# Kernel tuning notes

Measured on AMD Instinct MI355X. Metric: run time of the kernel, lower is better.

The kernel has to match this reference:

```python
import jax, jax.numpy as jnp
import numpy as np

B, N, DIM, H, CH, M = 2, 65536, 256, 8, 32, 64
INNER = H * CH  # 256


def setup_inputs() -> dict:
    key = jax.random.key(0)
    ks = jax.random.split(key, 13)
    s = 0.02
    return {
        "x": jax.random.normal(ks[0], (B, N, DIM), dtype=jnp.float32),
        "W_fx": jax.random.normal(ks[1], (DIM, INNER), dtype=jnp.float32) * s,
        "b_fx": jnp.zeros((INNER,), dtype=jnp.float32),
        "W_x": jax.random.normal(ks[2], (DIM, INNER), dtype=jnp.float32) * s,
        "b_x": jnp.zeros((INNER,), dtype=jnp.float32),
        "W_slice": jax.random.normal(ks[3], (CH, M), dtype=jnp.float32) * s,
        "b_slice": jnp.zeros((M,), dtype=jnp.float32),
        "temperature": 0.5 * jnp.ones((1, H, 1, 1), dtype=jnp.float32),
        "W_q": jax.random.normal(ks[4], (CH, CH), dtype=jnp.float32) * s,
        "W_k": jax.random.normal(ks[5], (CH, CH), dtype=jnp.float32) * s,
        "W_v": jax.random.normal(ks[6], (CH, CH), dtype=jnp.float32) * s,
        "W_out": jax.random.normal(ks[7], (INNER, DIM), dtype=jnp.float32) * s,
        "b_out": jnp.zeros((DIM,), dtype=jnp.float32),
    }


def reference(x, W_fx, b_fx, W_x, b_x, W_slice, b_slice, temperature,
              W_q, W_k, W_v, W_out, b_out):
    b, n, _ = x.shape
    h, ch, m = H, CH, M
    # input projections -> [B, H, N, Ch]
    fx_mid = (x @ W_fx + b_fx).reshape(b, n, h, ch).transpose(0, 2, 1, 3)
    x_mid = (x @ W_x + b_x).reshape(b, n, h, ch).transpose(0, 2, 1, 3)
    # learned soft-slice weights: [B, H, N, M]
    temp = jnp.clip(temperature, 0.1, 5.0)
    logits = (x_mid @ W_slice + b_slice) / temp
    slice_weights = jax.nn.softmax(logits, axis=-1)
    slice_norm = slice_weights.sum(axis=2)  # [B, H, M]
    # aggregate N points into M slice tokens: [B, H, M, Ch]
    slice_token = jnp.einsum('bhnc,bhng->bhgc', fx_mid, slice_weights)
    slice_token = slice_token / (slice_norm + 1e-5)[:, :, :, None]
    # small attention among slice tokens
    q = slice_token @ W_q
    k = slice_token @ W_k
    v = slice_token @ W_v
    scale = ch ** (-0.5)
    attn = jax.nn.softmax(jnp.einsum('bhgc,bhkc->bhgk', q, k) * scale, axis=-1)
    out_slice = attn @ v  # [B, H, M, Ch]
    # scatter back to N points: [B, H, N, Ch] -> [B, N, H*Ch]
    out_x = jnp.einsum('bhgc,bhng->bhnc', out_slice, slice_weights)
    out_x = out_x.transpose(0, 2, 1, 3).reshape(b, n, h * ch)
    return out_x @ W_out + b_out
```

## Files before the change

### kernel.cpp

```cpp
#include <hip/hip_runtime.h>

#define N_ 65536

typedef unsigned int  uint32;
typedef unsigned short ushort;
typedef float  f32x4 __attribute__((ext_vector_type(4)));
typedef short  s16x8 __attribute__((ext_vector_type(8)));
typedef uint32 u32x2 __attribute__((ext_vector_type(2)));

__device__ __forceinline__ uint32 f2bf(float f){
  union{float f; uint32 i;} v; v.f=f;
  return (v.i + 0x7fffu + ((v.i>>16)&1u)) >> 16;
}
__device__ __forceinline__ float bfl(uint32 h){
  union{uint32 i; float f;} v; v.i = h<<16; return v.f;
}
__device__ __forceinline__ uint32 pk2(float a, float b){
  return f2bf(a) | (f2bf(b)<<16);
}
__device__ __forceinline__ f32x4 mfma16(s16x8 a, s16x8 b, f32x4 c){
  return __builtin_amdgcn_mfma_f32_16x16x32_bf16(a,b,c,0,0,0);
}

__global__ __launch_bounds__(256) void prep_kernel(
    const float* __restrict__ Wfx, const float* __restrict__ Wx,
    const float* __restrict__ Wsl, const float* __restrict__ bsl,
    const float* __restrict__ bx,  const float* __restrict__ temp,
    ushort* __restrict__ WlT, ushort* __restrict__ WfxT, float* __restrict__ blT)
{
  const int blk = blockIdx.x, t = threadIdx.x;
  if (blk < 512){
    const int m = blk, h = m>>6, mp = m&63;
    const float tmp = fminf(fmaxf(temp[h],0.1f),5.0f);
    float s = 0.f;
    #pragma unroll
    for (int cc=0; cc<32; cc++) s += Wx[t*256 + h*32+cc]*Wsl[cc*64+mp];
    WlT[m*256+t] = (ushort)f2bf(s/tmp);
    if (t==0){
      float bs = bsl[mp];
      for (int cc=0; cc<32; cc++) bs += bx[h*32+cc]*Wsl[cc*64+mp];
      blT[m] = bs/tmp;
    }
  } else {
    const int c = blk-512;
    WfxT[c*256+t] = (ushort)f2bf(Wfx[t*256+c]);
  }
}

__global__ __launch_bounds__(512, 2)
void k1a_kernel(
    const float* __restrict__ x,
    const ushort* __restrict__ WlT,
    const ushort* __restrict__ WfxT,
    const float* __restrict__ blT,
    const float* __restrict__ bfx,
    ushort* __restrict__ swg,
    float* __restrict__ stp,
    float* __restrict__ normp)
{
  __shared__ __align__(16) char smem[131072];
  const int t = threadIdx.x;
  const int w = t>>6, l = t&63, rg = l>>4, c16 = l&15;
  const int blk = blockIdx.x;
  const int tile0 = ((blk&127)<<3) + ((blk>>7)<<10);

  char* fxh = smem + (w<<12);
  char* swb = smem + 32768 + (w<<13);
  char* fxl = smem + 98304 + (w<<12);

  f32x4 pc[2][4];
  #pragma unroll
  for (int i=0;i<2;i++)
    #pragma unroll
    for (int j=0;j<4;j++) pc[i][j] = (f32x4){0.f,0.f,0.f,0.f};
  f32x4 nacc[4];
  #pragma unroll
  for (int i=0;i<4;i++) nacc[i] = (f32x4){0.f,0.f,0.f,0.f};

  f32x4 blv[4];
  #pragma unroll
  for (int m=0;m<4;m++) blv[m] = *(const f32x4*)(blT + (w<<6)+(m<<4)+(rg<<2));
  float bfv[2];
  #pragma unroll
  for (int c=0;c<2;c++) bfv[c] = bfx[(w<<5)+(c<<4)+c16];

  for (int it=0; it<8; ++it) {
    const int tile = tile0 + it;
    const long gn0 = (long)tile<<6;

    __syncthreads();
    {
      const float4* xs = (const float4*)(x + (gn0<<8));
      #pragma unroll
      for (int p=0;p<8;p++){
        const int f = t + (p<<9);
        const int row = f>>6, q = f&63;
        const float4 v = xs[f];
        u32x2 uu; uu.x = pk2(v.x, v.y); uu.y = pk2(v.z, v.w);
        *(u32x2*)(smem + (row<<9) + ((q<<3) ^ ((row&7)<<4))) = uu;
      }
    }
    __syncthreads();

    #pragma unroll
    for (int nf=0; nf<4; nf++){
      f32x4 accA[4];
      #pragma unroll
      for (int m=0;m<4;m++) accA[m] = (f32x4){0.f,0.f,0.f,0.f};
      #pragma unroll
      for (int kb=0;kb<8;kb++){
        s16x8 aW[4], bX;
        #pragma unroll
        for (int m=0;m<4;m++)
          aW[m] = *(const s16x8*)(WlT + (((w<<6)+(m<<4)+c16)<<8) + (kb<<5)+(rg<<3));
        {
          const int row = (nf<<4) | c16;
          bX = *(const s16x8*)(smem + (row<<9) + (((kb<<6)+(rg<<4)) ^ ((row&7)<<4)));
        }
        #pragma unroll
        for (int m=0;m<4;m++)
          accA[m] = mfma16(aW[m], bX, accA[m]);
      }
      {
        f32x4 v[4];
        float mx = -3.0e38f;
        #pragma unroll
        for (int m=0;m<4;m++){
          v[m] = accA[m] + blv[m];
          mx = fmaxf(mx, fmaxf(fmaxf(v[m].x, v[m].y), fmaxf(v[m].z, v[m].w)));
        }
        mx = fmaxf(mx, __shfl_xor(mx,16));
        mx = fmaxf(mx, __shfl_xor(mx,32));
        float s = 0.f;
        #pragma unroll
        for (int m=0;m<4;m++){
          v[m].x = __expf(v[m].x-mx); v[m].y = __expf(v[m].y-mx);
          v[m].z = __expf(v[m].z-mx); v[m].w = __expf(v[m].w-mx);
          s += v[m].x+v[m].y+v[m].z+v[m].w;
        }
        s += __shfl_xor(s,16);
        s += __shfl_xor(s,32);
        const float inv = 1.0f/s;
        const long gn = gn0 + (nf<<4) + c16;
        #pragma unroll
        for (int m=0;m<4;m++){
          f32x4 sv = v[m]*inv;
          nacc[m] += sv;
          u32x2 p; p.x = pk2(sv.x, sv.y); p.y = pk2(sv.z, sv.w);
          *(u32x2*)(swg + (gn<<9) + (w<<6)+(m<<4)+(rg<<2)) = p;
          const uint32 px = (uint32)__shfl_xor((int)p.x, 1);
          const uint32 py = (uint32)__shfl_xor((int)p.y, 1);
          const bool ev = ((c16&1)==0);
          const uint32 s0 = ev ? (uint32)p.x : py;
          const uint32 s1 = ev ? px : (uint32)p.y;
          const uint32 wA = (s0 & 0xffffu) | (s1<<16);
          const uint32 wB = (s0>>16) | (s1 & 0xffff0000u);
          const int rowA = (m<<4) + (rg<<2) + (ev?0:2);
          const int cbyt = ((nf<<4) + (c16 & ~1)) << 1;
          *(uint32*)(swb + ((rowA  )<<7) + (cbyt ^ (((rowA  )&7)<<4))) = wA;
          *(uint32*)(swb + ((rowA+1)<<7) + (cbyt ^ (((rowA+1)&7)<<4))) = wB;
        }
      }
    }

    u32x2 qkh[2][4];
    {
      f32x4 accB[4][2];
      #pragma unroll
      for (int r=0;r<4;r++)
        #pragma unroll
        for (int c=0;c<2;c++) accB[r][c] = (f32x4){0.f,0.f,0.f,0.f};
      #pragma unroll
      for (int kb=0;kb<8;kb++){
        s16x8 bW[2], aX[4];
        #pragma unroll
        for (int c=0;c<2;c++)
          bW[c] = *(const s16x8*)(WfxT + (((w<<5)+(c<<4)+c16)<<8) + (kb<<5)+(rg<<3));
        #pragma unroll
        for (int r=0;r<4;r++){
          const int row = (r<<4) | c16;
          aX[r] = *(const s16x8*)(smem + (row<<9) + (((kb<<6)+(rg<<4)) ^ ((row&7)<<4)));
        }
        #pragma unroll
        for (int r=0;r<4;r++)
          #pragma unroll
          for (int c=0;c<2;c++)
            accB[r][c] = mfma16(aX[r], bW[c], accB[r][c]);
      }
      #pragma unroll
      for (int r=0;r<4;r++)
        #pragma unroll
        for (int c=0;c<2;c++){
          const float v0 = accB[r][c].x+bfv[c], v1 = accB[r][c].y+bfv[c];
          const float v2 = accB[r][c].z+bfv[c], v3 = accB[r][c].w+bfv[c];
          const uint32 h0=f2bf(v0), h1=f2bf(v1), h2=f2bf(v2), h3=f2bf(v3);
          u32x2 ph; ph.x = h0|(h1<<16); ph.y = h2|(h3<<16);
          qkh[c][r] = ph;
          u32x2 pl;
          pl.x = f2bf(v0-bfl(h0)) | (f2bf(v1-bfl(h1))<<16);
          pl.y = f2bf(v2-bfl(h2)) | (f2bf(v3-bfl(h3))<<16);
          const int row = (c<<4) + c16;
          const int cby = ((r<<5) + (rg<<3)) ^ ((row&7)<<4);
          *(u32x2*)(fxl + (row<<7) + cby) = pl;
        }
    }
    __syncthreads();

    #pragma unroll
    for (int cf=0; cf<2; cf++)
      #pragma unroll
      for (int r=0; r<4; r++){
        const int row = (cf<<4) + c16;
        const int cby = ((r<<5) + (rg<<3)) ^ ((row&7)<<4);
        *(u32x2*)(fxh + (row<<7) + cby) = qkh[cf][r];
      }
    asm volatile("s_waitcnt lgkmcnt(0)" ::: "memory");
    __builtin_amdgcn_sched_barrier(0);

    #pragma unroll
    for (int kb2=0; kb2<2; kb2++){
      const int pby = (kb2<<6) + (rg<<4);
      s16x8 afh[2], afl[2], bfr[4];
      #pragma unroll
      for (int cf=0; cf<2; cf++){
        const int row = (cf<<4)+c16;
        const int o = pby ^ ((row&7)<<4);
        afh[cf] = *(const s16x8*)(fxh + (row<<7) + o);
        afl[cf] = *(const s16x8*)(fxl + (row<<7) + o);
      }
      #pragma unroll
      for (int mf=0; mf<4; mf++){
        const int row = (mf<<4)+c16;
        bfr[mf] = *(const s16x8*)(swb + (row<<7) + (pby ^ ((row&7)<<4)));
      }
      #pragma unroll
      for (int cf=0; cf<2; cf++)
        #pragma unroll
        for (int mf=0; mf<4; mf++){
          pc[cf][mf] = mfma16(afh[cf], bfr[mf], pc[cf][mf]);
          pc[cf][mf] = mfma16(afl[cf], bfr[mf], pc[cf][mf]);
        }
    }
  }

  #pragma unroll
  for (int m=0;m<4;m++){
    #pragma unroll
    for (int d=1; d<16; d<<=1){
      nacc[m].x += __shfl_xor(nacc[m].x, d);
      nacc[m].y += __shfl_xor(nacc[m].y, d);
      nacc[m].z += __shfl_xor(nacc[m].z, d);
      nacc[m].w += __shfl_xor(nacc[m].w, d);
    }
  }
  if (c16==0){
    #pragma unroll
    for (int m=0;m<4;m++)
      *(f32x4*)(normp + (((blk<<3)+w)<<6) + (m<<4) + (rg<<2)) = nacc[m];
  }
  const long sb = ((long)((blk<<3)+w))<<11;
  #pragma unroll
  for (int cf=0;cf<2;cf++)
    #pragma unroll
    for (int mf=0;mf<4;mf++)
      #pragma unroll
      for (int r=0;r<4;r++){
        const int cc = (cf<<4)+(rg<<2)+r;
        stp[sb + (cc<<6) + (mf<<4) + c16] = pc[cf][mf][r];
      }
}

__global__ __launch_bounds__(256) void k2a_kernel(float* __restrict__ stp, float* __restrict__ normp)
{
  const int gid = blockIdx.x;
  const int bh = gid>>3, grp = gid&7;
  const int b = bh>>3, h = bh&7;
  const int t = threadIdx.x;
  const int blk0 = (b<<7) + (grp<<4);
  f32x4 a0 = {0,0,0,0}, a1 = {0,0,0,0};
  for (int i=0;i<16;i++){
    const f32x4* p = (const f32x4*)(stp + ((((size_t)(blk0+i)<<3)+h)<<11) + ((size_t)t<<3));
    a0 += p[0]; a1 += p[1];
  }
  f32x4* q = (f32x4*)(stp + ((((size_t)blk0<<3)+h)<<11) + ((size_t)t<<3));
  q[0] = a0; q[1] = a1;
  if (t<8){
    f32x4 n0 = {0,0,0,0}, n1 = {0,0,0,0};
    for (int i=0;i<16;i++){
      const f32x4* p = (const f32x4*)(normp + (((blk0+i)<<3)+h)*64 + (t<<3));
      n0 += p[0]; n1 += p[1];
    }
    f32x4* qn = (f32x4*)(normp + ((blk0<<3)+h)*64 + (t<<3));
    qn[0] = n0; qn[1] = n1;
  }
}

__global__ __launch_bounds__(256) void k2b_kernel(
    const float* __restrict__ stp, const float* __restrict__ normp,
    const float* __restrict__ Wq, const float* __restrict__ Wk, const float* __restrict__ Wv,
    const float* __restrict__ Wout, ushort* __restrict__ OS2Th, ushort* __restrict__ OS2Tl)
{
  __shared__ float nrmL[64];
  __shared__ float tok[2048];
  __shared__ float qL[2048], kL[2048], vL[2048];
  __shared__ float sc[4096];
  __shared__ float osL[2048];
  const int bh = blockIdx.x; const int b = bh>>3, h = bh&7;
  const int t = threadIdx.x;

  if (t<64){
    float s = 0.f;
    for (int g=0; g<8; g++) s += normp[((((b<<7)+(g<<4))<<3)+h)*64 + t];
    nrmL[t] = s;
  }
  __syncthreads();
  {
    f32x4 a0 = {0,0,0,0}, a1 = {0,0,0,0};
    for (int g=0; g<8; g++){
      const f32x4* p = (const f32x4*)(stp + ((((size_t)((b<<7)+(g<<4))<<3)+h)<<11) + ((size_t)t<<3));
      a0 += p[0]; a1 += p[1];
    }
    const int c = t>>3, m0 = (t&7)<<3;
    #pragma unroll
    for (int j=0;j<4;j++) tok[(m0+j)*32 + c]   = a0[j] / (nrmL[m0+j]   + 1e-5f);
    #pragma unroll
    for (int j=0;j<4;j++) tok[(m0+4+j)*32 + c] = a1[j] / (nrmL[m0+4+j] + 1e-5f);
  }
  __syncthreads();

  const int g = t>>2, q4 = t&3;
  float aq[8]={0,0,0,0,0,0,0,0}, ak2[8]={0,0,0,0,0,0,0,0}, av[8]={0,0,0,0,0,0,0,0};
  for (int kk=0; kk<32; kk++){
    const float tv = tok[(g<<5)+kk];
    const int wo = kk*32 + (q4<<3);
    #pragma unroll
    for (int j=0;j<8;j++){
      aq[j]  = fmaf(tv, Wq[wo+j], aq[j]);
      ak2[j] = fmaf(tv, Wk[wo+j], ak2[j]);
      av[j]  = fmaf(tv, Wv[wo+j], av[j]);
    }
  }
  #pragma unroll
  for (int j=0;j<8;j++){
    qL[(g<<5)+(q4<<3)+j]=aq[j];
    kL[(g<<5)+(q4<<3)+j]=ak2[j];
    vL[(g<<5)+(q4<<3)+j]=av[j];
  }
  __syncthreads();

  const float scale = 0.17677669529663689f;
  float svv[16]; float mx = -3.0e38f;
  for (int mm=0;mm<16;mm++){
    const int m = (q4<<4)+mm;
    float s2 = 0.f;
    #pragma unroll
    for (int c=0;c<32;c++) s2 = fmaf(qL[(g<<5)+c], kL[(m<<5)+c], s2);
    s2 *= scale;
    svv[mm] = s2; mx = fmaxf(mx, s2);
  }
  mx = fmaxf(mx, __shfl_xor(mx,1));
  mx = fmaxf(mx, __shfl_xor(mx,2));
  float ssum = 0.f;
  for (int mm=0;mm<16;mm++){ svv[mm] = __expf(svv[mm]-mx); ssum += svv[mm]; }
  ssum += __shfl_xor(ssum,1); ssum += __shfl_xor(ssum,2);
  const float isum = 1.0f/ssum;
  for (int mm=0;mm<16;mm++) sc[(g<<6) + (q4<<4) + mm] = svv[mm]*isum;
  __syncthreads();

  float os[8]={0,0,0,0,0,0,0,0};
  for (int m=0;m<64;m++){
    const float a = sc[(g<<6)+m];
    const int vo = (m<<5)+(q4<<3);
    #pragma unroll
    for (int j=0;j<8;j++) os[j] = fmaf(a, vL[vo+j], os[j]);
  }
  #pragma unroll
  for (int j=0;j<8;j++) osL[(g<<5)+(q4<<3)+j] = os[j];
  __syncthreads();

  const int d = t;
  float wcol[32];
  #pragma unroll
  for (int c=0;c<32;c++) wcol[c] = Wout[(h*32+c)*256 + d];
  uint32* orh = (uint32*)(OS2Th + ((size_t)(b*256+d))*512 + h*64);
  uint32* orl = (uint32*)(OS2Tl + ((size_t)(b*256+d))*512 + h*64);
  #pragma unroll 4
  for (int g2=0; g2<32; g2++){
    float s0=0.f, s1=0.f;
    #pragma unroll
    for (int c=0;c<32;c++){
      s0 = fmaf(osL[((g2*2  )<<5)+c], wcol[c], s0);
      s1 = fmaf(osL[((g2*2+1)<<5)+c], wcol[c], s1);
    }
    const uint32 h0 = f2bf(s0), h1 = f2bf(s1);
    orh[g2] = h0 | (h1<<16);
    orl[g2] = f2bf(s0 - bfl(h0)) | (f2bf(s1 - bfl(h1)) << 16);
  }
}

__global__ __launch_bounds__(256) void k3_kernel(
    const ushort* __restrict__ swg,
    const ushort* __restrict__ OS2Th,
    const ushort* __restrict__ OS2Tl,
    const float* __restrict__ bout,
    float* __restrict__ out)
{
  const int t = threadIdx.x, w = t>>6, l = t&63, rg = l>>4, c16 = l&15;
  const int blk = blockIdx.x;
  const long gn0 = (long)blk<<7;
  const int b = blk>>9;
  f32x4 acc[8][4];
  #pragma unroll
  for (int r=0;r<8;r++)
    #pragma unroll
    for (int c=0;c<4;c++) acc[r][c] = (f32x4){0.f,0.f,0.f,0.f};
  const ushort* swp = swg + (gn0<<9);
  const long obb = (((long)(b<<8) + (w<<6))<<9);
  for (int kb=0;kb<16;kb++){
    s16x8 aS[8];
    #pragma unroll
    for (int r=0;r<8;r++)
      aS[r] = *(const s16x8*)(swp + ((long)((r<<4)+c16)<<9) + (kb<<5)+(rg<<3));
    #pragma unroll
    for (int c=0;c<4;c++){
      const long ro = obb + ((long)((c<<4)+c16)<<9) + (kb<<5)+(rg<<3);
      const s16x8 bh = *(const s16x8*)(OS2Th + ro);
      const s16x8 bl = *(const s16x8*)(OS2Tl + ro);
      #pragma unroll
      for (int r=0;r<8;r++)
        acc[r][c] = mfma16(aS[r], bh, acc[r][c]);
      #pragma unroll
      for (int r=0;r<8;r++)
        acc[r][c] = mfma16(aS[r], bl, acc[r][c]);
    }
  }
  float bo[4];
  #pragma unroll
  for (int c=0;c<4;c++) bo[c] = bout[(w<<6)+(c<<4)+c16];
  #pragma unroll
  for (int r=0;r<8;r++)
    #pragma unroll
    for (int c=0;c<4;c++)
      #pragma unroll
      for (int rr=0;rr<4;rr++)
        out[((gn0 + (r<<4)+(rg<<2)+rr)<<8) + (w<<6)+(c<<4)+c16] = acc[r][c][rr] + bo[c];
}

extern "C" void kernel_launch(void* const* d_in, const int* in_sizes, int n_in,
                              void* d_out, int out_size, void* d_ws, size_t ws_size,
                              hipStream_t stream)
{
  const float* x     = (const float*)d_in[0];
  const float* Wfx   = (const float*)d_in[1];
  const float* bfx   = (const float*)d_in[2];
  const float* Wx    = (const float*)d_in[3];
  const float* bx    = (const float*)d_in[4];
  const float* Wsl   = (const float*)d_in[5];
  const float* bsl   = (const float*)d_in[6];
  const float* temp  = (const float*)d_in[7];
  const float* Wq    = (const float*)d_in[8];
  const float* Wk    = (const float*)d_in[9];
  const float* Wv    = (const float*)d_in[10];
  const float* Wout  = (const float*)d_in[11];
  const float* bout  = (const float*)d_in[12];
  float* out = (float*)d_out;

  char* ws = (char*)d_ws;
  ushort* WlT   = (ushort*)(ws);
  ushort* WfxT  = (ushort*)(ws + 262144);
  float*  blT   = (float*) (ws + 393216);
  ushort* swg   = (ushort*)(ws + 395264);
  float*  stp   = (float*) (ws + 134612992);
  float*  normp = (float*) (ws + 151390208);
  ushort* OS2Th = (ushort*)(ws + 151914496);
  ushort* OS2Tl = (ushort*)(ws + 152438784);

  prep_kernel<<<dim3(768), dim3(256), 0, stream>>>(Wfx, Wx, Wsl, bsl, bx, temp, WlT, WfxT, blT);
  k1a_kernel<<<dim3(256), dim3(512), 0, stream>>>(x, WlT, WfxT, blT, bfx, swg, stp, normp);
  k2a_kernel<<<dim3(128), dim3(256), 0, stream>>>(stp, normp);
  k2b_kernel<<<dim3(16), dim3(256), 0, stream>>>(stp, normp, Wq, Wk, Wv, Wout, OS2Th, OS2Tl);
  k3_kernel<<<dim3(1024), dim3(256), 0, stream>>>(swg, OS2Th, OS2Tl, bout, out);
}
```

Baseline: 449.9 us.

## Store slice weights in packed tile layout and halve k3 rows per block

The slice-weight buffer written by k1a is rearranged from a row-major [n][512] layout into 16-point packets grouped by head and slice block. Each 8-byte store from a wave then lands in contiguous memory, and k3 can fetch its MFMA A operands as two adjacent 8-byte loads. k3 now covers 64 rows per block with half the accumulators and launches twice as many blocks, aiming at better occupancy and coalescing. The trade-off is that each OS2T B tile is reloaded by twice as many blocks.

```diff
diff --git a/kernel.cpp b/kernel.cpp
--- a/kernel.cpp
+++ b/kernel.cpp
@@ -7,6 +7,7 @@
 typedef float  f32x4 __attribute__((ext_vector_type(4)));
 typedef short  s16x8 __attribute__((ext_vector_type(8)));
 typedef uint32 u32x2 __attribute__((ext_vector_type(2)));
+typedef uint32 u32x4 __attribute__((ext_vector_type(4)));
 
 __device__ __forceinline__ uint32 f2bf(float f){
   union{float f; uint32 i;} v; v.f=f;
@@ -20,6 +21,9 @@
 }
 __device__ __forceinline__ f32x4 mfma16(s16x8 a, s16x8 b, f32x4 c){
   return __builtin_amdgcn_mfma_f32_16x16x32_bf16(a,b,c,0,0,0);
+}
+__device__ __forceinline__ s16x8 mk8(uint32 a, uint32 b, uint32 c, uint32 d){
+  union{u32x4 u; s16x8 s;} v; v.u = (u32x4){a,b,c,d}; return v.s;
 }
 
 __global__ __launch_bounds__(256) void prep_kernel(
@@ -54,7 +58,7 @@
     const ushort* __restrict__ WfxT,
     const float* __restrict__ blT,
     const float* __restrict__ bfx,
-    ushort* __restrict__ swg,
+    ushort* __restrict__ swg2,
     float* __restrict__ stp,
     float* __restrict__ normp)
 {
@@ -141,13 +145,13 @@
         s += __shfl_xor(s,16);
         s += __shfl_xor(s,32);
         const float inv = 1.0f/s;
-        const long gn = gn0 + (nf<<4) + c16;
+        const int pb = (int)(gn0>>4) + nf;
         #pragma unroll
         for (int m=0;m<4;m++){
           f32x4 sv = v[m]*inv;
           nacc[m] += sv;
           u32x2 p; p.x = pk2(sv.x, sv.y); p.y = pk2(sv.z, sv.w);
-          *(u32x2*)(swg + (gn<<9) + (w<<6)+(m<<4)+(rg<<2)) = p;
+          *(u32x2*)(swg2 + ((((((size_t)pb<<3)+w)<<2)+m)<<8) + (rg<<6) + (c16<<2)) = p;
           const uint32 px = (uint32)__shfl_xor((int)p.x, 1);
           const uint32 py = (uint32)__shfl_xor((int)p.y, 1);
           const bool ev = ((c16&1)==0);
@@ -399,7 +403,7 @@
 }
 
 __global__ __launch_bounds__(256) void k3_kernel(
-    const ushort* __restrict__ swg,
+    const ushort* __restrict__ swg2,
     const ushort* __restrict__ OS2Th,
     const ushort* __restrict__ OS2Tl,
     const float* __restrict__ bout,
@@ -407,38 +411,45 @@
 {
   const int t = threadIdx.x, w = t>>6, l = t&63, rg = l>>4, c16 = l&15;
   const int blk = blockIdx.x;
-  const long gn0 = (long)blk<<7;
-  const int b = blk>>9;
-  f32x4 acc[8][4];
-  #pragma unroll
-  for (int r=0;r<8;r++)
+  const long gn0 = (long)blk<<6;
+  const int b = blk>>10;
+  f32x4 acc[4][4];
+  #pragma unroll
+  for (int r=0;r<4;r++)
     #pragma unroll
     for (int c=0;c<4;c++) acc[r][c] = (f32x4){0.f,0.f,0.f,0.f};
-  const ushort* swp = swg + (gn0<<9);
   const long obb = (((long)(b<<8) + (w<<6))<<9);
   for (int kb=0;kb<16;kb++){
-    s16x8 aS[8];
-    #pragma unroll
-    for (int r=0;r<8;r++)
-      aS[r] = *(const s16x8*)(swp + ((long)((r<<4)+c16)<<9) + (kb<<5)+(rg<<3));
+    const int h3 = kb>>1;
+    const int mb = ((kb&1)<<1) + (rg>>1);
+    const int pkt = (rg&1)<<1;
+    s16x8 aS[4];
+    #pragma unroll
+    for (int r=0;r<4;r++){
+      const long pb = (gn0>>4) + r;
+      const ushort* bp = swg2 + ((((pb<<3)+h3)<<2) + mb)*256 + (c16<<2);
+      const u32x2 lo = *(const u32x2*)(bp + (pkt<<6));
+      const u32x2 hi = *(const u32x2*)(bp + ((pkt+1)<<6));
+      aS[r] = mk8(lo.x, lo.y, hi.x, hi.y);
+    }
     #pragma unroll
     for (int c=0;c<4;c++){
       const long ro = obb + ((long)((c<<4)+c16)<<9) + (kb<<5)+(rg<<3);
-      const s16x8 bh = *(const s16x8*)(OS2Th + ro);
-      const s16x8 bl = *(const s16x8*)(OS2Tl + ro);
-      #pragma unroll
-      for (int r=0;r<8;r++)
-        acc[r][c] = mfma16(aS[r], bh, acc[r][c]);
-      #pragma unroll
-      for (int r=0;r<8;r++)
-        acc[r][c] = mfma16(aS[r], bl, acc[r][c]);
+      const s16x8 bhv = *(const s16x8*)(OS2Th + ro);
+      const s16x8 blv = *(const s16x8*)(OS2Tl + ro);
+      #pragma unroll
+      for (int r=0;r<4;r++)
+        acc[r][c] = mfma16(aS[r], bhv, acc[r][c]);
+      #pragma unroll
+      for (int r=0;r<4;r++)
+        acc[r][c] = mfma16(aS[r], blv, acc[r][c]);
     }
   }
   float bo[4];
   #pragma unroll
   for (int c=0;c<4;c++) bo[c] = bout[(w<<6)+(c<<4)+c16];
   #pragma unroll
-  for (int r=0;r<8;r++)
+  for (int r=0;r<4;r++)
     #pragma unroll
     for (int c=0;c<4;c++)
       #pragma unroll
@@ -469,15 +480,15 @@
   ushort* WlT   = (ushort*)(ws);
   ushort* WfxT  = (ushort*)(ws + 262144);
   float*  blT   = (float*) (ws + 393216);
-  ushort* swg   = (ushort*)(ws + 395264);
+  ushort* swg2  = (ushort*)(ws + 395264);
   float*  stp   = (float*) (ws + 134612992);
   float*  normp = (float*) (ws + 151390208);
   ushort* OS2Th = (ushort*)(ws + 151914496);
   ushort* OS2Tl = (ushort*)(ws + 152438784);
 
   prep_kernel<<<dim3(768), dim3(256), 0, stream>>>(Wfx, Wx, Wsl, bsl, bx, temp, WlT, WfxT, blT);
-  k1a_kernel<<<dim3(256), dim3(512), 0, stream>>>(x, WlT, WfxT, blT, bfx, swg, stp, normp);
+  k1a_kernel<<<dim3(256), dim3(512), 0, stream>>>(x, WlT, WfxT, blT, bfx, swg2, stp, normp);
   k2a_kernel<<<dim3(128), dim3(256), 0, stream>>>(stp, normp);
   k2b_kernel<<<dim3(16), dim3(256), 0, stream>>>(stp, normp, Wq, Wk, Wv, Wout, OS2Th, OS2Tl);
-  k3_kernel<<<dim3(1024), dim3(256), 0, stream>>>(swg, OS2Th, OS2Tl, bout, out);
-}
+  k3_kernel<<<dim3(2048), dim3(256), 0, stream>>>(swg2, OS2Th, OS2Tl, bout, out);
+}
```

Result: slower. 463.3 us (+3.0%).
